# Kernel tuning notes

Measured on AMD Instinct MI355X. Metric: run time of the kernel, lower is better.

Reference implementation:

```python
import jax, jax.numpy as jnp
import numpy as np

TOP_K = 2  # config.num_experts_per_tok


def setup_inputs() -> dict:
    key = jax.random.key(0)
    ks = jax.random.split(key, 5)
    B, S, H, F, E = 1, 2048, 2048, 1408, 8
    sc_h = 1.0 / np.sqrt(H)
    sc_f = 1.0 / np.sqrt(F)
    return {
        "hidden_states": jax.random.normal(ks[0], (B, S, H), jnp.float32),
        "gate_w": jax.random.normal(ks[1], (E, H), jnp.float32) * sc_h,
        "w1": jax.random.normal(ks[2], (E, F, H), jnp.float32) * sc_h,
        "w3": jax.random.normal(ks[3], (E, F, H), jnp.float32) * sc_h,
        "w2": jax.random.normal(ks[4], (E, H, F), jnp.float32) * sc_f,
    }


def reference(hidden_states, gate_w, w1, w3, w2):
    B, S, H = hidden_states.shape
    x = hidden_states.reshape(-1, H)            # [T, H]
    T = x.shape[0]
    E = gate_w.shape[0]

    # Router: logits -> fp32 softmax -> top-k -> renormalize
    router_logits = x @ gate_w.T                # [T, E]
    probs = jax.nn.softmax(router_logits.astype(jnp.float32), axis=-1)
    topk_w, topk_idx = jax.lax.top_k(probs, TOP_K)          # [T, K]
    topk_w = topk_w / topk_w.sum(axis=-1, keepdims=True)
    topk_w = topk_w.astype(x.dtype)

    # Scatter top-k weights into a dense [T, E] combine matrix (zero elsewhere)
    w_full = jnp.zeros((T, E), x.dtype).at[jnp.arange(T)[:, None], topk_idx].add(topk_w)

    # Per-expert SwiGLU MLP applied to all tokens; masked combine honors routing.
    g = jnp.einsum('th,efh->etf', x, w1)        # [E, T, F]
    u = jnp.einsum('th,efh->etf', x, w3)        # [E, T, F]
    h = jax.nn.silu(g) * u                      # [E, T, F]
    y = jnp.einsum('etf,ehf->eth', h, w2)       # [E, T, H]
    out = jnp.einsum('eth,te->th', y, w_full)   # [T, H]

    final_hidden_states = out.reshape(B, S, H)
    return final_hidden_states, router_logits
```

## Files before the change

kernel.cpp:

```cpp
#include <hip/hip_runtime.h>
#include <hip/hip_bf16.h>

#define T_TOK 2048
#define H_DIM 2048
#define F_DIM 1408
#define N_EXP 8
#define BM 128
#define BN 64
#define BK 64

#define NITEM 40
#define G1_NY (F_DIM / BN)
#define G2_NY (H_DIM / BN)
#define G1_CHUNK ((NITEM * G1_NY) / 8)
#define G2_CHUNK ((NITEM * G2_NY) / 8)

typedef float f32x4 __attribute__((ext_vector_type(4)));
typedef short s16x8 __attribute__((ext_vector_type(8)));

#define LOFF(row, kbyte) (((row) << 7) + ((kbyte) ^ (((row) & 7) << 4)))

__device__ __forceinline__ int bf2i(__hip_bfloat162 h) {
  int r; __builtin_memcpy(&r, &h, 4); return r;
}

__device__ __forceinline__ int4 pack8(float4 a, float4 b) {
  int4 r;
  r.x = bf2i(__float22bfloat162_rn(float2{a.x, a.y}));
  r.y = bf2i(__float22bfloat162_rn(float2{a.z, a.w}));
  r.z = bf2i(__float22bfloat162_rn(float2{b.x, b.y}));
  r.w = bf2i(__float22bfloat162_rn(float2{b.z, b.w}));
  return r;
}

__device__ __forceinline__ unsigned short f2bf(float f) {
  __hip_bfloat16 h = __float2bfloat16(f);
  unsigned short r; __builtin_memcpy(&r, &h, 2); return r;
}

__device__ __forceinline__ f32x4 mfma16(s16x8 a, s16x8 b, f32x4 c) {
  return __builtin_amdgcn_mfma_f32_16x16x32_bf16(a, b, c, 0, 0, 0);
}

__global__ void router_kernel(const float* __restrict__ x, const float* __restrict__ gw,
                              float* __restrict__ logits, int* __restrict__ tk_idx,
                              float* __restrict__ tk_w, unsigned short* __restrict__ xb) {
  __shared__ float xs[H_DIM];
  __shared__ float lg[N_EXP];
  const int t = blockIdx.x;
  const int tid = threadIdx.x;
  const float4 xv = ((const float4*)(x + (size_t)t * H_DIM))[tid];
  ((float4*)xs)[tid] = xv;
  int2 cw;
  cw.x = bf2i(__float22bfloat162_rn(float2{xv.x, xv.y}));
  cw.y = bf2i(__float22bfloat162_rn(float2{xv.z, xv.w}));
  ((int2*)(xb + (size_t)t * H_DIM))[tid] = cw;
  __syncthreads();
  const int w = tid >> 6, l = tid & 63;
  const float* g = gw + w * H_DIM;
  float s = 0.f;
  for (int j = l; j < H_DIM; j += 64) s += xs[j] * g[j];
#pragma unroll
  for (int o = 32; o; o >>= 1) s += __shfl_down(s, o);
  if (l == 0) lg[w] = s;
  __syncthreads();
  if (tid == 0) {
    float mx = lg[0];
#pragma unroll
    for (int i = 1; i < N_EXP; i++) mx = fmaxf(mx, lg[i]);
    float p[N_EXP];
#pragma unroll
    for (int i = 0; i < N_EXP; i++) p[i] = __expf(lg[i] - mx);
    int i0 = 0;
#pragma unroll
    for (int i = 1; i < N_EXP; i++) if (p[i] > p[i0]) i0 = i;
    int i1 = (i0 == 0) ? 1 : 0;
#pragma unroll
    for (int i = 0; i < N_EXP; i++) if (i != i0 && p[i] > p[i1]) i1 = i;
    const float ww = p[i0] + p[i1];
    tk_idx[t * 2] = i0; tk_idx[t * 2 + 1] = i1;
    tk_w[t * 2] = p[i0] / ww; tk_w[t * 2 + 1] = p[i1] / ww;
#pragma unroll
    for (int i = 0; i < N_EXP; i++) logits[t * N_EXP + i] = lg[i];
  }
}

__global__ void build_lists(const int* __restrict__ tk_idx, const float* __restrict__ tk_w,
                            int* __restrict__ counts, int* __restrict__ entries,
                            float* __restrict__ wlist) {
  const int e = blockIdx.x;
  const int l = threadIdx.x;
  int base = 0;
  for (int t0 = 0; t0 < T_TOK; t0 += 64) {
    const int t = t0 + l;
    int sel = -1; float w = 0.f;
    const int i0 = tk_idx[t * 2], i1 = tk_idx[t * 2 + 1];
    if (i0 == e) { sel = t * 2; w = tk_w[t * 2]; }
    else if (i1 == e) { sel = t * 2 + 1; w = tk_w[t * 2 + 1]; }
    const unsigned long long mask = __ballot(sel >= 0);
    const int pos = base + __popcll(mask & ((1ull << l) - 1ull));
    if (sel >= 0) { entries[e * T_TOK + pos] = sel; wlist[e * T_TOK + pos] = w; }
    base += __popcll(mask);
  }
  if (l == 0) counts[e] = base;
}

__global__ void build_items(const int* __restrict__ counts, int* __restrict__ items) {
  if (threadIdx.x == 0) {
    int n = 0;
#pragma unroll
    for (int e = 0; e < N_EXP; e++) {
      const int c = counts[e];
      for (int m0 = 0; m0 < c; m0 += BM) items[1 + n++] = (e << 16) | (m0 / BM);
    }
    items[0] = n;
  }
}

#define G1_STEP(SA, SB1, SB3, VA0, VA1, B10, B11, B30, B31, KNEXT)            \
  {                                                                           \
    *(int4*)((SA) + offA0) = VA0;                                             \
    *(int4*)((SA) + offA1) = VA1;                                             \
    *(int4*)((SB1) + offB) = pack8(B10, B11);                                 \
    *(int4*)((SB3) + offB) = pack8(B30, B31);                                 \
    const int kn = (KNEXT);                                                   \
    VA0 = *(const int4*)(pa0 + kn);                                           \
    VA1 = *(const int4*)(pa1 + kn);                                           \
    B10 = *(const float4*)(pb1 + kn);                                         \
    B11 = *(const float4*)(pb1 + kn + 4);                                     \
    B30 = *(const float4*)(pb3 + kn);                                         \
    B31 = *(const float4*)(pb3 + kn + 4);                                     \
    asm volatile("s_waitcnt lgkmcnt(0)" ::: "memory");                        \
    __builtin_amdgcn_s_barrier();                                             \
    _Pragma("unroll")                                                         \
    for (int kk = 0; kk < 2; kk++) {                                          \
      const int kbyte = kk * 64 + kb;                                         \
      const s16x8 a0 = *(const s16x8*)((SA) + LOFF(rowA0, kbyte));            \
      const s16x8 a1 = *(const s16x8*)((SA) + LOFF(rowA1, kbyte));            \
      const s16x8 p0 = *(const s16x8*)((SB1) + LOFF(rowB0, kbyte));           \
      const s16x8 p1 = *(const s16x8*)((SB1) + LOFF(rowB1, kbyte));           \
      const s16x8 q0 = *(const s16x8*)((SB3) + LOFF(rowB0, kbyte));           \
      const s16x8 q1 = *(const s16x8*)((SB3) + LOFF(rowB1, kbyte));           \
      aG[0][0] = mfma16(a0, p0, aG[0][0]); aG[0][1] = mfma16(a0, p1, aG[0][1]); \
      aG[1][0] = mfma16(a1, p0, aG[1][0]); aG[1][1] = mfma16(a1, p1, aG[1][1]); \
      aU[0][0] = mfma16(a0, q0, aU[0][0]); aU[0][1] = mfma16(a0, q1, aU[0][1]); \
      aU[1][0] = mfma16(a1, q0, aU[1][0]); aU[1][1] = mfma16(a1, q1, aU[1][1]); \
    }                                                                         \
  }

__global__ __launch_bounds__(512)
void moe_gemm1(const float* __restrict__ w1, const float* __restrict__ w3,
               const unsigned short* __restrict__ xb,
               const int* __restrict__ counts, const int* __restrict__ entries,
               const int* __restrict__ items,
               unsigned short* __restrict__ hb) {
  const int lin = blockIdx.x;
  const int virt = (lin & 7) * G1_CHUNK + (lin >> 3);
  const int ix = virt % NITEM;
  const int iy = virt / NITEM;
  if (ix >= items[0]) return;
  const int it = items[1 + ix];
  const int e = it >> 16;
  const int m0 = (it & 0xffff) * BM;
  const int cnt = counts[e];
  const int rem = cnt - m0;
  const int n0 = iy * BN;

  __shared__ unsigned short sA[2][BM * BK];
  __shared__ unsigned short sB1[2][BN * BK];
  __shared__ unsigned short sB3[2][BN * BK];
  char* sA0c = (char*)sA[0]; char* sA1c = (char*)sA[1];
  char* sB10c = (char*)sB1[0]; char* sB11c = (char*)sB1[1];
  char* sB30c = (char*)sB3[0]; char* sB31c = (char*)sB3[1];

  const int tid = threadIdx.x;
  const int lane = tid & 63;
  const int wave = tid >> 6;
  const int wm = wave >> 1, wn = wave & 1;

  const int* elist = entries + e * T_TOK + m0;

  const int r0 = tid >> 3;
  const int gc = tid & 7;
  const int ra1 = r0 + 64;
  const int tok0 = elist[r0 < rem ? r0 : 0] >> 1;
  const int tok1 = elist[ra1 < rem ? ra1 : 0] >> 1;
  const unsigned short* pa0 = xb + (size_t)tok0 * H_DIM + gc * 8;
  const unsigned short* pa1 = xb + (size_t)tok1 * H_DIM + gc * 8;
  const float* pb1 = w1 + ((size_t)e * F_DIM + n0 + r0) * H_DIM + gc * 8;
  const float* pb3 = w3 + ((size_t)e * F_DIM + n0 + r0) * H_DIM + gc * 8;
  const int offA0 = LOFF(r0, gc * 16);
  const int offA1 = LOFF(ra1, gc * 16);
  const int offB = LOFF(r0, gc * 16);

  const int rowA0 = wm * 32 + (lane & 15);
  const int rowA1 = rowA0 + 16;
  const int rowB0 = wn * 32 + (lane & 15);
  const int rowB1 = rowB0 + 16;
  const int kb = (lane >> 4) * 16;

  const f32x4 zero = {0.f, 0.f, 0.f, 0.f};
  f32x4 aG[2][2], aU[2][2];
#pragma unroll
  for (int i = 0; i < 2; i++)
#pragma unroll
    for (int j = 0; j < 2; j++) { aG[i][j] = zero; aU[i][j] = zero; }

  int4 Pa0 = *(const int4*)(pa0), Pa1 = *(const int4*)(pa1);
  float4 Pb10 = *(const float4*)(pb1), Pb11 = *(const float4*)(pb1 + 4);
  float4 Pb30 = *(const float4*)(pb3), Pb31 = *(const float4*)(pb3 + 4);
  int4 Qa0 = *(const int4*)(pa0 + BK), Qa1 = *(const int4*)(pa1 + BK);
  float4 Qb10 = *(const float4*)(pb1 + BK), Qb11 = *(const float4*)(pb1 + BK + 4);
  float4 Qb30 = *(const float4*)(pb3 + BK), Qb31 = *(const float4*)(pb3 + BK + 4);

  const int NT1 = H_DIM / BK;
  for (int t = 0; t < NT1; t += 2) {
    const int kp = (t + 2 < NT1) ? (t + 2) * BK : 0;
    const int kq = (t + 3 < NT1) ? (t + 3) * BK : 0;
    G1_STEP(sA0c, sB10c, sB30c, Pa0, Pa1, Pb10, Pb11, Pb30, Pb31, kp);
    G1_STEP(sA1c, sB11c, sB31c, Qa0, Qa1, Qb10, Qb11, Qb30, Qb31, kq);
  }

#pragma unroll
  for (int i = 0; i < 2; i++) {
#pragma unroll
    for (int r = 0; r < 4; r++) {
      const int m = wm * 32 + i * 16 + ((lane >> 4) << 2) + r;
      if (m < rem) {
        const int entry = elist[m];
        unsigned short* hp = hb + (size_t)entry * F_DIM + n0 + wn * 32 + (lane & 15);
#pragma unroll
        for (int j = 0; j < 2; j++) {
          const float g = aG[i][j][r];
          const float u = aU[i][j][r];
          const float s = g / (1.f + __expf(-g)) * u;
          hp[j * 16] = f2bf(s);
        }
      }
    }
  }
}

#define G2_STEP(SA, SB, VA0, VA1, B0, B1, KNEXT)                              \
  {                                                                           \
    *(int4*)((SA) + offA0) = VA0;                                             \
    *(int4*)((SA) + offA1) = VA1;                                             \
    *(int4*)((SB) + offB) = pack8(B0, B1);                                    \
    const int kn = (KNEXT);                                                   \
    VA0 = *(const int4*)(pa0 + kn);                                           \
    VA1 = *(const int4*)(pa1 + kn);                                           \
    B0 = *(const float4*)(pb + kn);                                           \
    B1 = *(const float4*)(pb + kn + 4);                                       \
    asm volatile("s_waitcnt lgkmcnt(0)" ::: "memory");                        \
    __builtin_amdgcn_s_barrier();                                             \
    _Pragma("unroll")                                                         \
    for (int kk = 0; kk < 2; kk++) {                                          \
      const int kbyte = kk * 64 + kb;                                         \
      const s16x8 a0 = *(const s16x8*)((SA) + LOFF(rowA0, kbyte));            \
      const s16x8 a1 = *(const s16x8*)((SA) + LOFF(rowA1, kbyte));            \
      const s16x8 f0 = *(const s16x8*)((SB) + LOFF(rowB0, kbyte));            \
      const s16x8 f1 = *(const s16x8*)((SB) + LOFF(rowB1, kbyte));            \
      ac[0][0] = mfma16(a0, f0, ac[0][0]); ac[0][1] = mfma16(a0, f1, ac[0][1]); \
      ac[1][0] = mfma16(a1, f0, ac[1][0]); ac[1][1] = mfma16(a1, f1, ac[1][1]); \
    }                                                                         \
  }

__global__ __launch_bounds__(512)
void moe_gemm2(const float* __restrict__ w2,
               const unsigned short* __restrict__ hb,
               const int* __restrict__ counts, const int* __restrict__ entries,
               const float* __restrict__ wlist, const int* __restrict__ items,
               float* __restrict__ out) {
  const int lin = blockIdx.x;
  const int virt = (lin & 7) * G2_CHUNK + (lin >> 3);
  const int ix = virt % NITEM;
  const int iy = virt / NITEM;
  if (ix >= items[0]) return;
  const int it = items[1 + ix];
  const int e = it >> 16;
  const int m0 = (it & 0xffff) * BM;
  const int cnt = counts[e];
  const int rem = cnt - m0;
  const int n0 = iy * BN;

  __shared__ unsigned short sA[2][BM * BK];
  __shared__ unsigned short sB[2][BN * BK];
  char* sA0c = (char*)sA[0]; char* sA1c = (char*)sA[1];
  char* sB0c = (char*)sB[0]; char* sB1c = (char*)sB[1];

  const int tid = threadIdx.x;
  const int lane = tid & 63;
  const int wave = tid >> 6;
  const int wm = wave >> 1, wn = wave & 1;

  const int* elist = entries + e * T_TOK + m0;
  const float* wl = wlist + e * T_TOK + m0;

  const int r0 = tid >> 3;
  const int gc = tid & 7;
  const int ra1 = r0 + 64;
  const int en0 = elist[r0 < rem ? r0 : 0];
  const int en1 = elist[ra1 < rem ? ra1 : 0];
  const unsigned short* pa0 = hb + (size_t)en0 * F_DIM + gc * 8;
  const unsigned short* pa1 = hb + (size_t)en1 * F_DIM + gc * 8;
  const float* pb = w2 + ((size_t)e * H_DIM + n0 + r0) * F_DIM + gc * 8;
  const int offA0 = LOFF(r0, gc * 16);
  const int offA1 = LOFF(ra1, gc * 16);
  const int offB = LOFF(r0, gc * 16);

  const int rowA0 = wm * 32 + (lane & 15);
  const int rowA1 = rowA0 + 16;
  const int rowB0 = wn * 32 + (lane & 15);
  const int rowB1 = rowB0 + 16;
  const int kb = (lane >> 4) * 16;

  const f32x4 zero = {0.f, 0.f, 0.f, 0.f};
  f32x4 ac[2][2];
#pragma unroll
  for (int i = 0; i < 2; i++)
#pragma unroll
    for (int j = 0; j < 2; j++) ac[i][j] = zero;

  int4 Pa0 = *(const int4*)(pa0), Pa1 = *(const int4*)(pa1);
  float4 Pb0 = *(const float4*)(pb), Pb1 = *(const float4*)(pb + 4);
  int4 Qa0 = *(const int4*)(pa0 + BK), Qa1 = *(const int4*)(pa1 + BK);
  float4 Qb0 = *(const float4*)(pb + BK), Qb1 = *(const float4*)(pb + BK + 4);

  const int NT2 = F_DIM / BK;
  for (int t = 0; t < NT2; t += 2) {
    const int kp = (t + 2 < NT2) ? (t + 2) * BK : 0;
    const int kq = (t + 3 < NT2) ? (t + 3) * BK : 0;
    G2_STEP(sA0c, sB0c, Pa0, Pa1, Pb0, Pb1, kp);
    G2_STEP(sA1c, sB1c, Qa0, Qa1, Qb0, Qb1, kq);
  }

#pragma unroll
  for (int i = 0; i < 2; i++) {
#pragma unroll
    for (int r = 0; r < 4; r++) {
      const int m = wm * 32 + i * 16 + ((lane >> 4) << 2) + r;
      if (m < rem) {
        const int entry = elist[m];
        const int t = entry >> 1;
        const float wgt = wl[m];
        float* op = out + (size_t)t * H_DIM + n0 + wn * 32 + (lane & 15);
#pragma unroll
        for (int j = 0; j < 2; j++) atomicAdd(op + j * 16, wgt * ac[i][j][r]);
      }
    }
  }
}

extern "C" void kernel_launch(void* const* d_in, const int* in_sizes, int n_in,
                              void* d_out, int out_size, void* d_ws, size_t ws_size,
                              hipStream_t stream) {
  const float* x  = (const float*)d_in[0];
  const float* gw = (const float*)d_in[1];
  const float* w1 = (const float*)d_in[2];
  const float* w3 = (const float*)d_in[3];
  const float* w2 = (const float*)d_in[4];
  float* out = (float*)d_out;
  float* logits = out + (size_t)T_TOK * H_DIM;

  char* ws = (char*)d_ws;
  size_t off = 0;
  unsigned short* xb = (unsigned short*)(ws + off); off += (size_t)T_TOK * H_DIM * 2;
  unsigned short* hb = (unsigned short*)(ws + off); off += (size_t)T_TOK * 2 * F_DIM * 2;
  int*   tk_idx = (int*)(ws + off);   off += (size_t)T_TOK * 2 * 4;
  float* tk_w   = (float*)(ws + off); off += (size_t)T_TOK * 2 * 4;
  int*   counts = (int*)(ws + off);   off += 256;
  int*   entries = (int*)(ws + off);  off += (size_t)N_EXP * T_TOK * 4;
  float* wlist  = (float*)(ws + off); off += (size_t)N_EXP * T_TOK * 4;
  int*   items  = (int*)(ws + off);   off += 256;

  (void)hipMemsetAsync(d_out, 0, (size_t)out_size * sizeof(float), stream);
  router_kernel<<<dim3(T_TOK), 512, 0, stream>>>(x, gw, logits, tk_idx, tk_w, xb);
  build_lists<<<dim3(N_EXP), 64, 0, stream>>>(tk_idx, tk_w, counts, entries, wlist);
  build_items<<<dim3(1), 64, 0, stream>>>(counts, items);
  moe_gemm1<<<dim3(NITEM * G1_NY), 512, 0, stream>>>(w1, w3, xb, counts, entries, items, hb);
  moe_gemm2<<<dim3(NITEM * G2_NY), 512, 0, stream>>>(w2, hb, counts, entries, wlist, items, out);
}
```

Before: 238.5 us.

## Switch GEMMs to single LDS buffer with one-tile register prefetch

Both MoE GEMM kernels move from double-buffered shared memory with a two-tile-deep register prefetch to a single shared buffer with a one-tile-deep register prefetch, adding an extra barrier before each LDS store. This halves LDS use per block and cuts register pressure from holding two in-flight global tiles, which may allow more blocks per CU. In exchange, every k-step now needs two barriers and global loads have less lead time before they are consumed, so latency hiding may get worse.

```diff
diff --git a/kernel.cpp b/kernel.cpp
--- a/kernel.cpp
+++ b/kernel.cpp
@@ -117,30 +117,32 @@
   }
 }
 
-#define G1_STEP(SA, SB1, SB3, VA0, VA1, B10, B11, B30, B31, KNEXT)            \
+#define G1_STEP(VA0, VA1, B10, B11, B30, B31, WA0, WA1, WB10, WB11, WB30, WB31, KNEXT) \
   {                                                                           \
-    *(int4*)((SA) + offA0) = VA0;                                             \
-    *(int4*)((SA) + offA1) = VA1;                                             \
-    *(int4*)((SB1) + offB) = pack8(B10, B11);                                 \
-    *(int4*)((SB3) + offB) = pack8(B30, B31);                                 \
+    asm volatile("s_waitcnt lgkmcnt(0)" ::: "memory");                        \
+    __builtin_amdgcn_s_barrier();                                             \
+    *(int4*)(sAc + offA0) = VA0;                                              \
+    *(int4*)(sAc + offA1) = VA1;                                              \
+    *(int4*)(sB1c + offB) = pack8(B10, B11);                                  \
+    *(int4*)(sB3c + offB) = pack8(B30, B31);                                  \
     const int kn = (KNEXT);                                                   \
-    VA0 = *(const int4*)(pa0 + kn);                                           \
-    VA1 = *(const int4*)(pa1 + kn);                                           \
-    B10 = *(const float4*)(pb1 + kn);                                         \
-    B11 = *(const float4*)(pb1 + kn + 4);                                     \
-    B30 = *(const float4*)(pb3 + kn);                                         \
-    B31 = *(const float4*)(pb3 + kn + 4);                                     \
+    WA0 = *(const int4*)(pa0 + kn);                                           \
+    WA1 = *(const int4*)(pa1 + kn);                                           \
+    WB10 = *(const float4*)(pb1 + kn);                                        \
+    WB11 = *(const float4*)(pb1 + kn + 4);                                    \
+    WB30 = *(const float4*)(pb3 + kn);                                        \
+    WB31 = *(const float4*)(pb3 + kn + 4);                                    \
     asm volatile("s_waitcnt lgkmcnt(0)" ::: "memory");                        \
     __builtin_amdgcn_s_barrier();                                             \
     _Pragma("unroll")                                                         \
     for (int kk = 0; kk < 2; kk++) {                                          \
       const int kbyte = kk * 64 + kb;                                         \
-      const s16x8 a0 = *(const s16x8*)((SA) + LOFF(rowA0, kbyte));            \
-      const s16x8 a1 = *(const s16x8*)((SA) + LOFF(rowA1, kbyte));            \
-      const s16x8 p0 = *(const s16x8*)((SB1) + LOFF(rowB0, kbyte));           \
-      const s16x8 p1 = *(const s16x8*)((SB1) + LOFF(rowB1, kbyte));           \
-      const s16x8 q0 = *(const s16x8*)((SB3) + LOFF(rowB0, kbyte));           \
-      const s16x8 q1 = *(const s16x8*)((SB3) + LOFF(rowB1, kbyte));           \
+      const s16x8 a0 = *(const s16x8*)(sAc + LOFF(rowA0, kbyte));             \
+      const s16x8 a1 = *(const s16x8*)(sAc + LOFF(rowA1, kbyte));             \
+      const s16x8 p0 = *(const s16x8*)(sB1c + LOFF(rowB0, kbyte));            \
+      const s16x8 p1 = *(const s16x8*)(sB1c + LOFF(rowB1, kbyte));            \
+      const s16x8 q0 = *(const s16x8*)(sB3c + LOFF(rowB0, kbyte));            \
+      const s16x8 q1 = *(const s16x8*)(sB3c + LOFF(rowB1, kbyte));            \
       aG[0][0] = mfma16(a0, p0, aG[0][0]); aG[0][1] = mfma16(a0, p1, aG[0][1]); \
       aG[1][0] = mfma16(a1, p0, aG[1][0]); aG[1][1] = mfma16(a1, p1, aG[1][1]); \
       aU[0][0] = mfma16(a0, q0, aU[0][0]); aU[0][1] = mfma16(a0, q1, aU[0][1]); \
@@ -166,12 +168,10 @@
   const int rem = cnt - m0;
   const int n0 = iy * BN;
 
-  __shared__ unsigned short sA[2][BM * BK];
-  __shared__ unsigned short sB1[2][BN * BK];
-  __shared__ unsigned short sB3[2][BN * BK];
-  char* sA0c = (char*)sA[0]; char* sA1c = (char*)sA[1];
-  char* sB10c = (char*)sB1[0]; char* sB11c = (char*)sB1[1];
-  char* sB30c = (char*)sB3[0]; char* sB31c = (char*)sB3[1];
+  __shared__ unsigned short sA[BM * BK];
+  __shared__ unsigned short sB1[BN * BK];
+  __shared__ unsigned short sB3[BN * BK];
+  char* sAc = (char*)sA; char* sB1c = (char*)sB1; char* sB3c = (char*)sB3;
 
   const int tid = threadIdx.x;
   const int lane = tid & 63;
@@ -209,16 +209,15 @@
   int4 Pa0 = *(const int4*)(pa0), Pa1 = *(const int4*)(pa1);
   float4 Pb10 = *(const float4*)(pb1), Pb11 = *(const float4*)(pb1 + 4);
   float4 Pb30 = *(const float4*)(pb3), Pb31 = *(const float4*)(pb3 + 4);
-  int4 Qa0 = *(const int4*)(pa0 + BK), Qa1 = *(const int4*)(pa1 + BK);
-  float4 Qb10 = *(const float4*)(pb1 + BK), Qb11 = *(const float4*)(pb1 + BK + 4);
-  float4 Qb30 = *(const float4*)(pb3 + BK), Qb31 = *(const float4*)(pb3 + BK + 4);
+  int4 Qa0, Qa1;
+  float4 Qb10, Qb11, Qb30, Qb31;
 
   const int NT1 = H_DIM / BK;
   for (int t = 0; t < NT1; t += 2) {
+    const int kq = (t + 1 < NT1) ? (t + 1) * BK : 0;
     const int kp = (t + 2 < NT1) ? (t + 2) * BK : 0;
-    const int kq = (t + 3 < NT1) ? (t + 3) * BK : 0;
-    G1_STEP(sA0c, sB10c, sB30c, Pa0, Pa1, Pb10, Pb11, Pb30, Pb31, kp);
-    G1_STEP(sA1c, sB11c, sB31c, Qa0, Qa1, Qb10, Qb11, Qb30, Qb31, kq);
+    G1_STEP(Pa0, Pa1, Pb10, Pb11, Pb30, Pb31, Qa0, Qa1, Qb10, Qb11, Qb30, Qb31, kq);
+    G1_STEP(Qa0, Qa1, Qb10, Qb11, Qb30, Qb31, Pa0, Pa1, Pb10, Pb11, Pb30, Pb31, kp);
   }
 
 #pragma unroll
@@ -241,25 +240,27 @@
   }
 }
 
-#define G2_STEP(SA, SB, VA0, VA1, B0, B1, KNEXT)                              \
+#define G2_STEP(VA0, VA1, B0, B1, WA0, WA1, WB0, WB1, KNEXT)                  \
   {                                                                           \
-    *(int4*)((SA) + offA0) = VA0;                                             \
-    *(int4*)((SA) + offA1) = VA1;                                             \
-    *(int4*)((SB) + offB) = pack8(B0, B1);                                    \
+    asm volatile("s_waitcnt lgkmcnt(0)" ::: "memory");                        \
+    __builtin_amdgcn_s_barrier();                                             \
+    *(int4*)(sAc + offA0) = VA0;                                              \
+    *(int4*)(sAc + offA1) = VA1;                                              \
+    *(int4*)(sBc + offB) = pack8(B0, B1);                                     \
     const int kn = (KNEXT);                                                   \
-    VA0 = *(const int4*)(pa0 + kn);                                           \
-    VA1 = *(const int4*)(pa1 + kn);                                           \
-    B0 = *(const float4*)(pb + kn);                                           \
-    B1 = *(const float4*)(pb + kn + 4);                                       \
+    WA0 = *(const int4*)(pa0 + kn);                                           \
+    WA1 = *(const int4*)(pa1 + kn);                                           \
+    WB0 = *(const float4*)(pb + kn);                                          \
+    WB1 = *(const float4*)(pb + kn + 4);                                      \
     asm volatile("s_waitcnt lgkmcnt(0)" ::: "memory");                        \
     __builtin_amdgcn_s_barrier();                                             \
     _Pragma("unroll")                                                         \
     for (int kk = 0; kk < 2; kk++) {                                          \
       const int kbyte = kk * 64 + kb;                                         \
-      const s16x8 a0 = *(const s16x8*)((SA) + LOFF(rowA0, kbyte));            \
-      const s16x8 a1 = *(const s16x8*)((SA) + LOFF(rowA1, kbyte));            \
-      const s16x8 f0 = *(const s16x8*)((SB) + LOFF(rowB0, kbyte));            \
-      const s16x8 f1 = *(const s16x8*)((SB) + LOFF(rowB1, kbyte));            \
+      const s16x8 a0 = *(const s16x8*)(sAc + LOFF(rowA0, kbyte));             \
+      const s16x8 a1 = *(const s16x8*)(sAc + LOFF(rowA1, kbyte));             \
+      const s16x8 f0 = *(const s16x8*)(sBc + LOFF(rowB0, kbyte));             \
+      const s16x8 f1 = *(const s16x8*)(sBc + LOFF(rowB1, kbyte));             \
       ac[0][0] = mfma16(a0, f0, ac[0][0]); ac[0][1] = mfma16(a0, f1, ac[0][1]); \
       ac[1][0] = mfma16(a1, f0, ac[1][0]); ac[1][1] = mfma16(a1, f1, ac[1][1]); \
     }                                                                         \
@@ -283,10 +284,9 @@
   const int rem = cnt - m0;
   const int n0 = iy * BN;
 
-  __shared__ unsigned short sA[2][BM * BK];
-  __shared__ unsigned short sB[2][BN * BK];
-  char* sA0c = (char*)sA[0]; char* sA1c = (char*)sA[1];
-  char* sB0c = (char*)sB[0]; char* sB1c = (char*)sB[1];
+  __shared__ unsigned short sA[BM * BK];
+  __shared__ unsigned short sB[BN * BK];
+  char* sAc = (char*)sA; char* sBc = (char*)sB;
 
   const int tid = threadIdx.x;
   const int lane = tid & 63;
@@ -323,15 +323,15 @@
 
   int4 Pa0 = *(const int4*)(pa0), Pa1 = *(const int4*)(pa1);
   float4 Pb0 = *(const float4*)(pb), Pb1 = *(const float4*)(pb + 4);
-  int4 Qa0 = *(const int4*)(pa0 + BK), Qa1 = *(const int4*)(pa1 + BK);
-  float4 Qb0 = *(const float4*)(pb + BK), Qb1 = *(const float4*)(pb + BK + 4);
+  int4 Qa0, Qa1;
+  float4 Qb0, Qb1;
 
   const int NT2 = F_DIM / BK;
   for (int t = 0; t < NT2; t += 2) {
+    const int kq = (t + 1 < NT2) ? (t + 1) * BK : 0;
     const int kp = (t + 2 < NT2) ? (t + 2) * BK : 0;
-    const int kq = (t + 3 < NT2) ? (t + 3) * BK : 0;
-    G2_STEP(sA0c, sB0c, Pa0, Pa1, Pb0, Pb1, kp);
-    G2_STEP(sA1c, sB1c, Qa0, Qa1, Qb0, Qb1, kq);
+    G2_STEP(Pa0, Pa1, Pb0, Pb1, Qa0, Qa1, Qb0, Qb1, kq);
+    G2_STEP(Qa0, Qa1, Qb0, Qb1, Pa0, Pa1, Pb0, Pb1, kp);
   }
 
 #pragma unroll
```

Measured after the change: 246.1 us. 1.03x slower.

## Load gathered A operands directly to registers, drop A shared tiles, halve block size

Applied to the files above, without the earlier changes.

Both grouped GEMM kernels stop staging the gathered activation rows through shared memory. Each lane now loads its MFMA A fragments straight from global memory into registers, with one step of software prefetch. Blocks shrink from 512 to 256 threads, so each wave covers 64 rows instead of 32 and loads two weight rows per thread. This removes the A-tile LDS traffic and shared-memory footprint, and the barrier now sits before the B-tile stores. The cost is uncoalesced 16-byte global gathers of activations, more registers per thread, and fewer waves per block to hide latency.

```diff
diff --git a/kernel.cpp b/kernel.cpp
--- a/kernel.cpp
+++ b/kernel.cpp
@@ -117,38 +117,58 @@
   }
 }
 
-#define G1_STEP(SA, SB1, SB3, VA0, VA1, B10, B11, B30, B31, KNEXT)            \
+#define G1_STEP(SW1, SW3, SR1, SR3, A0C, A0N, KB_, KA_, KN_)                  \
   {                                                                           \
-    *(int4*)((SA) + offA0) = VA0;                                             \
-    *(int4*)((SA) + offA1) = VA1;                                             \
-    *(int4*)((SB1) + offB) = pack8(B10, B11);                                 \
-    *(int4*)((SB3) + offB) = pack8(B30, B31);                                 \
-    const int kn = (KNEXT);                                                   \
-    VA0 = *(const int4*)(pa0 + kn);                                           \
-    VA1 = *(const int4*)(pa1 + kn);                                           \
-    B10 = *(const float4*)(pb1 + kn);                                         \
-    B11 = *(const float4*)(pb1 + kn + 4);                                     \
-    B30 = *(const float4*)(pb3 + kn);                                         \
-    B31 = *(const float4*)(pb3 + kn + 4);                                     \
     asm volatile("s_waitcnt lgkmcnt(0)" ::: "memory");                        \
     __builtin_amdgcn_s_barrier();                                             \
+    *(int4*)((SW1) + offB0) = pack8(rb1[0][0], rb1[0][1]);                    \
+    *(int4*)((SW1) + offB1) = pack8(rb1[1][0], rb1[1][1]);                    \
+    *(int4*)((SW3) + offB0) = pack8(rb3[0][0], rb3[0][1]);                    \
+    *(int4*)((SW3) + offB1) = pack8(rb3[1][0], rb3[1][1]);                    \
+    {                                                                         \
+      const int kbl = (KB_);                                                  \
+      rb1[0][0] = *(const float4*)(pb1 + kbl);                                \
+      rb1[0][1] = *(const float4*)(pb1 + kbl + 4);                            \
+      rb1[1][0] = *(const float4*)(pb1 + rstep + kbl);                        \
+      rb1[1][1] = *(const float4*)(pb1 + rstep + kbl + 4);                    \
+      rb3[0][0] = *(const float4*)(pb3 + kbl);                                \
+      rb3[0][1] = *(const float4*)(pb3 + kbl + 4);                            \
+      rb3[1][0] = *(const float4*)(pb3 + rstep + kbl);                        \
+      rb3[1][1] = *(const float4*)(pb3 + rstep + kbl + 4);                    \
+    }                                                                         \
+    s16x8 a1[4];                                                              \
     _Pragma("unroll")                                                         \
-    for (int kk = 0; kk < 2; kk++) {                                          \
-      const int kbyte = kk * 64 + kb;                                         \
-      const s16x8 a0 = *(const s16x8*)((SA) + LOFF(rowA0, kbyte));            \
-      const s16x8 a1 = *(const s16x8*)((SA) + LOFF(rowA1, kbyte));            \
-      const s16x8 p0 = *(const s16x8*)((SB1) + LOFF(rowB0, kbyte));           \
-      const s16x8 p1 = *(const s16x8*)((SB1) + LOFF(rowB1, kbyte));           \
-      const s16x8 q0 = *(const s16x8*)((SB3) + LOFF(rowB0, kbyte));           \
-      const s16x8 q1 = *(const s16x8*)((SB3) + LOFF(rowB1, kbyte));           \
-      aG[0][0] = mfma16(a0, p0, aG[0][0]); aG[0][1] = mfma16(a0, p1, aG[0][1]); \
-      aG[1][0] = mfma16(a1, p0, aG[1][0]); aG[1][1] = mfma16(a1, p1, aG[1][1]); \
-      aU[0][0] = mfma16(a0, q0, aU[0][0]); aU[0][1] = mfma16(a0, q1, aU[0][1]); \
-      aU[1][0] = mfma16(a1, q0, aU[1][0]); aU[1][1] = mfma16(a1, q1, aU[1][1]); \
-    }                                                                         \
-  }
-
-__global__ __launch_bounds__(512)
+    for (int m = 0; m < 4; m++) {                                             \
+      A0N[m] = *(const s16x8*)(xb + aoff[m] + (KN_) + lk);                    \
+      a1[m] = *(const s16x8*)(xb + aoff[m] + (KA_) + 32 + lk);                \
+    }                                                                         \
+    {                                                                         \
+      const s16x8 b10 = *(const s16x8*)((SR1) + LOFF(rowB0, kb));             \
+      const s16x8 b11 = *(const s16x8*)((SR1) + LOFF(rowB1, kb));             \
+      const s16x8 b30 = *(const s16x8*)((SR3) + LOFF(rowB0, kb));             \
+      const s16x8 b31 = *(const s16x8*)((SR3) + LOFF(rowB1, kb));             \
+      _Pragma("unroll")                                                       \
+      for (int m = 0; m < 4; m++) {                                           \
+        aG[m][0] = mfma16(A0C[m], b10, aG[m][0]);                             \
+        aG[m][1] = mfma16(A0C[m], b11, aG[m][1]);                             \
+        aU[m][0] = mfma16(A0C[m], b30, aU[m][0]);                             \
+        aU[m][1] = mfma16(A0C[m], b31, aU[m][1]);                             \
+      }                                                                       \
+      const s16x8 c10 = *(const s16x8*)((SR1) + LOFF(rowB0, 64 + kb));        \
+      const s16x8 c11 = *(const s16x8*)((SR1) + LOFF(rowB1, 64 + kb));        \
+      const s16x8 c30 = *(const s16x8*)((SR3) + LOFF(rowB0, 64 + kb));        \
+      const s16x8 c31 = *(const s16x8*)((SR3) + LOFF(rowB1, 64 + kb));        \
+      _Pragma("unroll")                                                       \
+      for (int m = 0; m < 4; m++) {                                           \
+        aG[m][0] = mfma16(a1[m], c10, aG[m][0]);                              \
+        aG[m][1] = mfma16(a1[m], c11, aG[m][1]);                              \
+        aU[m][0] = mfma16(a1[m], c30, aU[m][0]);                              \
+        aU[m][1] = mfma16(a1[m], c31, aU[m][1]);                              \
+      }                                                                       \
+    }                                                                         \
+  }
+
+__global__ __launch_bounds__(256)
 void moe_gemm1(const float* __restrict__ w1, const float* __restrict__ w3,
                const unsigned short* __restrict__ xb,
                const int* __restrict__ counts, const int* __restrict__ entries,
@@ -162,16 +182,13 @@
   const int it = items[1 + ix];
   const int e = it >> 16;
   const int m0 = (it & 0xffff) * BM;
-  const int cnt = counts[e];
-  const int rem = cnt - m0;
+  const int rem = counts[e] - m0;
   const int n0 = iy * BN;
 
-  __shared__ unsigned short sA[2][BM * BK];
   __shared__ unsigned short sB1[2][BN * BK];
   __shared__ unsigned short sB3[2][BN * BK];
-  char* sA0c = (char*)sA[0]; char* sA1c = (char*)sA[1];
-  char* sB10c = (char*)sB1[0]; char* sB11c = (char*)sB1[1];
-  char* sB30c = (char*)sB3[0]; char* sB31c = (char*)sB3[1];
+  char* s1a = (char*)sB1[0]; char* s1b = (char*)sB1[1];
+  char* s3a = (char*)sB3[0]; char* s3b = (char*)sB3[1];
 
   const int tid = threadIdx.x;
   const int lane = tid & 63;
@@ -182,90 +199,113 @@
 
   const int r0 = tid >> 3;
   const int gc = tid & 7;
-  const int ra1 = r0 + 64;
-  const int tok0 = elist[r0 < rem ? r0 : 0] >> 1;
-  const int tok1 = elist[ra1 < rem ? ra1 : 0] >> 1;
-  const unsigned short* pa0 = xb + (size_t)tok0 * H_DIM + gc * 8;
-  const unsigned short* pa1 = xb + (size_t)tok1 * H_DIM + gc * 8;
   const float* pb1 = w1 + ((size_t)e * F_DIM + n0 + r0) * H_DIM + gc * 8;
   const float* pb3 = w3 + ((size_t)e * F_DIM + n0 + r0) * H_DIM + gc * 8;
-  const int offA0 = LOFF(r0, gc * 16);
-  const int offA1 = LOFF(ra1, gc * 16);
-  const int offB = LOFF(r0, gc * 16);
-
-  const int rowA0 = wm * 32 + (lane & 15);
-  const int rowA1 = rowA0 + 16;
-  const int rowB0 = wn * 32 + (lane & 15);
+  const size_t rstep = (size_t)32 * H_DIM;
+  const int offB0 = LOFF(r0, gc * 16);
+  const int offB1 = LOFF(r0 + 32, gc * 16);
+
+  const int lr = lane & 15;
+  const int lk = (lane >> 4) * 8;
+  int aoff[4];
+#pragma unroll
+  for (int m = 0; m < 4; m++) {
+    int q = wm * 64 + m * 16 + lr;
+    q = q < rem ? q : 0;
+    aoff[m] = (elist[q] >> 1) * H_DIM;
+  }
+
+  const int rowB0 = wn * 32 + lr;
   const int rowB1 = rowB0 + 16;
   const int kb = (lane >> 4) * 16;
 
   const f32x4 zero = {0.f, 0.f, 0.f, 0.f};
-  f32x4 aG[2][2], aU[2][2];
-#pragma unroll
-  for (int i = 0; i < 2; i++)
-#pragma unroll
-    for (int j = 0; j < 2; j++) { aG[i][j] = zero; aU[i][j] = zero; }
-
-  int4 Pa0 = *(const int4*)(pa0), Pa1 = *(const int4*)(pa1);
-  float4 Pb10 = *(const float4*)(pb1), Pb11 = *(const float4*)(pb1 + 4);
-  float4 Pb30 = *(const float4*)(pb3), Pb31 = *(const float4*)(pb3 + 4);
-  int4 Qa0 = *(const int4*)(pa0 + BK), Qa1 = *(const int4*)(pa1 + BK);
-  float4 Qb10 = *(const float4*)(pb1 + BK), Qb11 = *(const float4*)(pb1 + BK + 4);
-  float4 Qb30 = *(const float4*)(pb3 + BK), Qb31 = *(const float4*)(pb3 + BK + 4);
-
-  const int NT1 = H_DIM / BK;
-  for (int t = 0; t < NT1; t += 2) {
-    const int kp = (t + 2 < NT1) ? (t + 2) * BK : 0;
-    const int kq = (t + 3 < NT1) ? (t + 3) * BK : 0;
-    G1_STEP(sA0c, sB10c, sB30c, Pa0, Pa1, Pb10, Pb11, Pb30, Pb31, kp);
-    G1_STEP(sA1c, sB11c, sB31c, Qa0, Qa1, Qb10, Qb11, Qb30, Qb31, kq);
-  }
-
-#pragma unroll
-  for (int i = 0; i < 2; i++) {
+  f32x4 aG[4][2], aU[4][2];
+#pragma unroll
+  for (int m = 0; m < 4; m++) { aG[m][0] = zero; aG[m][1] = zero; aU[m][0] = zero; aU[m][1] = zero; }
+
+  float4 rb1[2][2], rb3[2][2];
+  rb1[0][0] = *(const float4*)(pb1);         rb1[0][1] = *(const float4*)(pb1 + 4);
+  rb1[1][0] = *(const float4*)(pb1 + rstep); rb1[1][1] = *(const float4*)(pb1 + rstep + 4);
+  rb3[0][0] = *(const float4*)(pb3);         rb3[0][1] = *(const float4*)(pb3 + 4);
+  rb3[1][0] = *(const float4*)(pb3 + rstep); rb3[1][1] = *(const float4*)(pb3 + rstep + 4);
+  *(int4*)(s1a + offB0) = pack8(rb1[0][0], rb1[0][1]);
+  *(int4*)(s1a + offB1) = pack8(rb1[1][0], rb1[1][1]);
+  *(int4*)(s3a + offB0) = pack8(rb3[0][0], rb3[0][1]);
+  *(int4*)(s3a + offB1) = pack8(rb3[1][0], rb3[1][1]);
+  rb1[0][0] = *(const float4*)(pb1 + BK);         rb1[0][1] = *(const float4*)(pb1 + BK + 4);
+  rb1[1][0] = *(const float4*)(pb1 + rstep + BK); rb1[1][1] = *(const float4*)(pb1 + rstep + BK + 4);
+  rb3[0][0] = *(const float4*)(pb3 + BK);         rb3[0][1] = *(const float4*)(pb3 + BK + 4);
+  rb3[1][0] = *(const float4*)(pb3 + rstep + BK); rb3[1][1] = *(const float4*)(pb3 + rstep + BK + 4);
+  s16x8 Pa0[4], Qa0[4];
+#pragma unroll
+  for (int m = 0; m < 4; m++) Pa0[m] = *(const s16x8*)(xb + aoff[m] + lk);
+
+  const int NT = H_DIM / BK;
+  for (int t = 0; t < NT; t += 2) {
+    const int kb2 = (t + 2 < NT) ? (t + 2) * BK : 0;
+    const int kb3 = (t + 3 < NT) ? (t + 3) * BK : 0;
+    G1_STEP(s1b, s3b, s1a, s3a, Pa0, Qa0, kb2, t * BK, (t + 1) * BK);
+    G1_STEP(s1a, s3a, s1b, s3b, Qa0, Pa0, kb3, (t + 1) * BK, kb2);
+  }
+
+#pragma unroll
+  for (int m = 0; m < 4; m++) {
 #pragma unroll
     for (int r = 0; r < 4; r++) {
-      const int m = wm * 32 + i * 16 + ((lane >> 4) << 2) + r;
-      if (m < rem) {
-        const int entry = elist[m];
-        unsigned short* hp = hb + (size_t)entry * F_DIM + n0 + wn * 32 + (lane & 15);
-#pragma unroll
-        for (int j = 0; j < 2; j++) {
-          const float g = aG[i][j][r];
-          const float u = aU[i][j][r];
-          const float s = g / (1.f + __expf(-g)) * u;
-          hp[j * 16] = f2bf(s);
+      const int mr = wm * 64 + m * 16 + (lane >> 4) * 4 + r;
+      if (mr < rem) {
+        const int entry = elist[mr];
+        unsigned short* hp = hb + (size_t)entry * F_DIM + n0 + wn * 32 + lr;
+#pragma unroll
+        for (int n = 0; n < 2; n++) {
+          const float g = aG[m][n][r];
+          const float u = aU[m][n][r];
+          hp[n * 16] = f2bf(g / (1.f + __expf(-g)) * u);
         }
       }
     }
   }
 }
 
-#define G2_STEP(SA, SB, VA0, VA1, B0, B1, KNEXT)                              \
+#define G2_STEP(SW, SR, A0C, A0N, KB_, KA_, KN_)                              \
   {                                                                           \
-    *(int4*)((SA) + offA0) = VA0;                                             \
-    *(int4*)((SA) + offA1) = VA1;                                             \
-    *(int4*)((SB) + offB) = pack8(B0, B1);                                    \
-    const int kn = (KNEXT);                                                   \
-    VA0 = *(const int4*)(pa0 + kn);                                           \
-    VA1 = *(const int4*)(pa1 + kn);                                           \
-    B0 = *(const float4*)(pb + kn);                                           \
-    B1 = *(const float4*)(pb + kn + 4);                                       \
     asm volatile("s_waitcnt lgkmcnt(0)" ::: "memory");                        \
     __builtin_amdgcn_s_barrier();                                             \
+    *(int4*)((SW) + offB0) = pack8(rb[0][0], rb[0][1]);                       \
+    *(int4*)((SW) + offB1) = pack8(rb[1][0], rb[1][1]);                       \
+    {                                                                         \
+      const int kbl = (KB_);                                                  \
+      rb[0][0] = *(const float4*)(pb + kbl);                                  \
+      rb[0][1] = *(const float4*)(pb + kbl + 4);                              \
+      rb[1][0] = *(const float4*)(pb + rstep + kbl);                          \
+      rb[1][1] = *(const float4*)(pb + rstep + kbl + 4);                      \
+    }                                                                         \
+    s16x8 a1[4];                                                              \
     _Pragma("unroll")                                                         \
-    for (int kk = 0; kk < 2; kk++) {                                          \
-      const int kbyte = kk * 64 + kb;                                         \
-      const s16x8 a0 = *(const s16x8*)((SA) + LOFF(rowA0, kbyte));            \
-      const s16x8 a1 = *(const s16x8*)((SA) + LOFF(rowA1, kbyte));            \
-      const s16x8 f0 = *(const s16x8*)((SB) + LOFF(rowB0, kbyte));            \
-      const s16x8 f1 = *(const s16x8*)((SB) + LOFF(rowB1, kbyte));            \
-      ac[0][0] = mfma16(a0, f0, ac[0][0]); ac[0][1] = mfma16(a0, f1, ac[0][1]); \
-      ac[1][0] = mfma16(a1, f0, ac[1][0]); ac[1][1] = mfma16(a1, f1, ac[1][1]); \
-    }                                                                         \
-  }
-
-__global__ __launch_bounds__(512)
+    for (int m = 0; m < 4; m++) {                                             \
+      A0N[m] = *(const s16x8*)(hb + aoff[m] + (KN_) + lk);                    \
+      a1[m] = *(const s16x8*)(hb + aoff[m] + (KA_) + 32 + lk);                \
+    }                                                                         \
+    {                                                                         \
+      const s16x8 b0 = *(const s16x8*)((SR) + LOFF(rowB0, kb));               \
+      const s16x8 b1 = *(const s16x8*)((SR) + LOFF(rowB1, kb));               \
+      _Pragma("unroll")                                                       \
+      for (int m = 0; m < 4; m++) {                                           \
+        ac[m][0] = mfma16(A0C[m], b0, ac[m][0]);                              \
+        ac[m][1] = mfma16(A0C[m], b1, ac[m][1]);                              \
+      }                                                                       \
+      const s16x8 c0 = *(const s16x8*)((SR) + LOFF(rowB0, 64 + kb));          \
+      const s16x8 c1 = *(const s16x8*)((SR) + LOFF(rowB1, 64 + kb));          \
+      _Pragma("unroll")                                                       \
+      for (int m = 0; m < 4; m++) {                                           \
+        ac[m][0] = mfma16(a1[m], c0, ac[m][0]);                               \
+        ac[m][1] = mfma16(a1[m], c1, ac[m][1]);                               \
+      }                                                                       \
+    }                                                                         \
+  }
+
+__global__ __launch_bounds__(256)
 void moe_gemm2(const float* __restrict__ w2,
                const unsigned short* __restrict__ hb,
                const int* __restrict__ counts, const int* __restrict__ entries,
@@ -279,14 +319,11 @@
   const int it = items[1 + ix];
   const int e = it >> 16;
   const int m0 = (it & 0xffff) * BM;
-  const int cnt = counts[e];
-  const int rem = cnt - m0;
+  const int rem = counts[e] - m0;
   const int n0 = iy * BN;
 
-  __shared__ unsigned short sA[2][BM * BK];
   __shared__ unsigned short sB[2][BN * BK];
-  char* sA0c = (char*)sA[0]; char* sA1c = (char*)sA[1];
-  char* sB0c = (char*)sB[0]; char* sB1c = (char*)sB[1];
+  char* sa = (char*)sB[0]; char* sb = (char*)sB[1];
 
   const int tid = threadIdx.x;
   const int lane = tid & 63;
@@ -298,54 +335,61 @@
 
   const int r0 = tid >> 3;
   const int gc = tid & 7;
-  const int ra1 = r0 + 64;
-  const int en0 = elist[r0 < rem ? r0 : 0];
-  const int en1 = elist[ra1 < rem ? ra1 : 0];
-  const unsigned short* pa0 = hb + (size_t)en0 * F_DIM + gc * 8;
-  const unsigned short* pa1 = hb + (size_t)en1 * F_DIM + gc * 8;
   const float* pb = w2 + ((size_t)e * H_DIM + n0 + r0) * F_DIM + gc * 8;
-  const int offA0 = LOFF(r0, gc * 16);
-  const int offA1 = LOFF(ra1, gc * 16);
-  const int offB = LOFF(r0, gc * 16);
-
-  const int rowA0 = wm * 32 + (lane & 15);
-  const int rowA1 = rowA0 + 16;
-  const int rowB0 = wn * 32 + (lane & 15);
+  const size_t rstep = (size_t)32 * F_DIM;
+  const int offB0 = LOFF(r0, gc * 16);
+  const int offB1 = LOFF(r0 + 32, gc * 16);
+
+  const int lr = lane & 15;
+  const int lk = (lane >> 4) * 8;
+  int aoff[4];
+#pragma unroll
+  for (int m = 0; m < 4; m++) {
+    int q = wm * 64 + m * 16 + lr;
+    q = q < rem ? q : 0;
+    aoff[m] = elist[q] * F_DIM;
+  }
+
+  const int rowB0 = wn * 32 + lr;
   const int rowB1 = rowB0 + 16;
   const int kb = (lane >> 4) * 16;
 
   const f32x4 zero = {0.f, 0.f, 0.f, 0.f};
-  f32x4 ac[2][2];
-#pragma unroll
-  for (int i = 0; i < 2; i++)
-#pragma unroll
-    for (int j = 0; j < 2; j++) ac[i][j] = zero;
-
-  int4 Pa0 = *(const int4*)(pa0), Pa1 = *(const int4*)(pa1);
-  float4 Pb0 = *(const float4*)(pb), Pb1 = *(const float4*)(pb + 4);
-  int4 Qa0 = *(const int4*)(pa0 + BK), Qa1 = *(const int4*)(pa1 + BK);
-  float4 Qb0 = *(const float4*)(pb + BK), Qb1 = *(const float4*)(pb + BK + 4);
-
-  const int NT2 = F_DIM / BK;
-  for (int t = 0; t < NT2; t += 2) {
-    const int kp = (t + 2 < NT2) ? (t + 2) * BK : 0;
-    const int kq = (t + 3 < NT2) ? (t + 3) * BK : 0;
-    G2_STEP(sA0c, sB0c, Pa0, Pa1, Pb0, Pb1, kp);
-    G2_STEP(sA1c, sB1c, Qa0, Qa1, Qb0, Qb1, kq);
-  }
-
-#pragma unroll
-  for (int i = 0; i < 2; i++) {
+  f32x4 ac[4][2];
+#pragma unroll
+  for (int m = 0; m < 4; m++) { ac[m][0] = zero; ac[m][1] = zero; }
+
+  float4 rb[2][2];
+  rb[0][0] = *(const float4*)(pb);         rb[0][1] = *(const float4*)(pb + 4);
+  rb[1][0] = *(const float4*)(pb + rstep); rb[1][1] = *(const float4*)(pb + rstep + 4);
+  *(int4*)(sa + offB0) = pack8(rb[0][0], rb[0][1]);
+  *(int4*)(sa + offB1) = pack8(rb[1][0], rb[1][1]);
+  rb[0][0] = *(const float4*)(pb + BK);         rb[0][1] = *(const float4*)(pb + BK + 4);
+  rb[1][0] = *(const float4*)(pb + rstep + BK); rb[1][1] = *(const float4*)(pb + rstep + BK + 4);
+  s16x8 Pa0[4], Qa0[4];
+#pragma unroll
+  for (int m = 0; m < 4; m++) Pa0[m] = *(const s16x8*)(hb + aoff[m] + lk);
+
+  const int NT = F_DIM / BK;
+  for (int t = 0; t < NT; t += 2) {
+    const int kb2 = (t + 2 < NT) ? (t + 2) * BK : 0;
+    const int kb3 = (t + 3 < NT) ? (t + 3) * BK : 0;
+    G2_STEP(sb, sa, Pa0, Qa0, kb2, t * BK, (t + 1) * BK);
+    G2_STEP(sa, sb, Qa0, Pa0, kb3, (t + 1) * BK, kb2);
+  }
+
+#pragma unroll
+  for (int m = 0; m < 4; m++) {
 #pragma unroll
     for (int r = 0; r < 4; r++) {
-      const int m = wm * 32 + i * 16 + ((lane >> 4) << 2) + r;
-      if (m < rem) {
-        const int entry = elist[m];
-        const int t = entry >> 1;
-        const float wgt = wl[m];
-        float* op = out + (size_t)t * H_DIM + n0 + wn * 32 + (lane & 15);
-#pragma unroll
-        for (int j = 0; j < 2; j++) atomicAdd(op + j * 16, wgt * ac[i][j][r]);
+      const int mr = wm * 64 + m * 16 + (lane >> 4) * 4 + r;
+      if (mr < rem) {
+        const int entry = elist[mr];
+        const int tok = entry >> 1;
+        const float wgt = wl[mr];
+        float* op = out + (size_t)tok * H_DIM + n0 + wn * 32 + lr;
+#pragma unroll
+        for (int n = 0; n < 2; n++) atomicAdd(op + n * 16, wgt * ac[m][n][r]);
       }
     }
   }
@@ -377,6 +421,6 @@
   router_kernel<<<dim3(T_TOK), 512, 0, stream>>>(x, gw, logits, tk_idx, tk_w, xb);
   build_lists<<<dim3(N_EXP), 64, 0, stream>>>(tk_idx, tk_w, counts, entries, wlist);
   build_items<<<dim3(1), 64, 0, stream>>>(counts, items);
-  moe_gemm1<<<dim3(NITEM * G1_NY), 512, 0, stream>>>(w1, w3, xb, counts, entries, items, hb);
-  moe_gemm2<<<dim3(NITEM * G2_NY), 512, 0, stream>>>(w2, hb, counts, entries, wlist, items, out);
-}
+  moe_gemm1<<<dim3(NITEM * G1_NY), 256, 0, stream>>>(w1, w3, xb, counts, entries, items, hb);
+  moe_gemm2<<<dim3(NITEM * G2_NY), 256, 0, stream>>>(w2, hb, counts, entries, wlist, items, out);
+}
```

Result: slower. 665.5 us (+179.0%).
